# Performance work log

Hardware: AMD Instinct MI355X
Metric: run time of the kernel (lower is better)

Reference implementation:

```python
import jax, jax.numpy as jnp
import numpy as np


def setup_inputs() -> dict:
    key0 = jax.random.key(0)
    k1, k2, k3 = jax.random.split(key0, 3)
    B, T, QS, KS = 64, 4096, 1024, 1024
    query = jax.random.normal(k1, (B, QS), dtype=jnp.float32)
    key = jax.random.normal(k2, (B, T, KS), dtype=jnp.float32)
    mask = jnp.ones((B, T), dtype=jnp.float32)
    # learned params: weights ~ U(-0.1, 0.1), bias zeros
    W = jax.random.uniform(k3, (KS, QS), dtype=jnp.float32) * 0.2 - 0.1
    bias = jnp.zeros((1,), dtype=jnp.float32)
    return {"query": query, "key": key, "mask": mask, "W": W, "bias": bias}


def reference(query, key, mask, W, bias):
    # mids[b] = W @ query[b]  -> [B, KS]
    mids = jnp.einsum("kq,bq->bk", W, query)
    # scores[b,t] = tanh(key[b,t] . mids[b] + bias)  -> [B, T]
    scores = jnp.tanh(jnp.einsum("btk,bk->bt", key, mids) + bias[0])
    # masked softmax over time dim (dim=1)
    scores = scores - jnp.max(scores, axis=1, keepdims=True)
    scores = jnp.exp(scores) * mask
    attn_weights = scores / jnp.sum(scores, axis=1, keepdims=True)
    return attn_weights
```

## Files before the change

### kernel.cpp

```cpp
#include <hip/hip_runtime.h>
#include <math.h>

#define BB 64
#define TT 4096
#define KSZ 1024
#define QSZ 1024

__global__ __launch_bounds__(256) void mids_kernel(const float* __restrict__ query,
                                                   const float* __restrict__ W,
                                                   float* __restrict__ mids) {
    const int bid  = blockIdx.x;
    const int b    = bid >> 6;
    const int kt   = bid & 63;
    const int lane = threadIdx.x & 63;
    const int wave = threadIdx.x >> 6;

    const float4* q4 = (const float4*)(query + (size_t)b * QSZ);
    float4 qr[4];
#pragma unroll
    for (int c = 0; c < 4; ++c) qr[c] = q4[lane + c * 64];

#pragma unroll
    for (int i = 0; i < 4; ++i) {
        const int k = kt * 16 + wave * 4 + i;
        const float4* w4 = (const float4*)(W + (size_t)k * QSZ);
        float sum = 0.f;
#pragma unroll
        for (int c = 0; c < 4; ++c) {
            float4 wv = w4[lane + c * 64];
            sum += wv.x * qr[c].x + wv.y * qr[c].y + wv.z * qr[c].z + wv.w * qr[c].w;
        }
#pragma unroll
        for (int off = 32; off > 0; off >>= 1) sum += __shfl_xor(sum, off, 64);
        if (lane == 0) mids[b * KSZ + k] = sum;
    }
}

__global__ __launch_bounds__(256) void scores_kernel(const float* __restrict__ key,
                                                     const float* __restrict__ mids,
                                                     const float* __restrict__ bias,
                                                     float* __restrict__ scores) {
    const int bid  = blockIdx.x;
    const int b    = bid >> 8;
    const int tt   = bid & 255;
    const int lane = threadIdx.x & 63;
    const int wave = threadIdx.x >> 6;

    const float4* m4 = (const float4*)(mids + (size_t)b * KSZ);
    float4 mr[4];
#pragma unroll
    for (int c = 0; c < 4; ++c) mr[c] = m4[lane + c * 64];
    const float bv = bias[0];

#pragma unroll
    for (int i = 0; i < 4; ++i) {
        const int t = tt * 16 + wave * 4 + i;
        const float4* k4 = (const float4*)(key + ((size_t)b * TT + t) * KSZ);
        float sum = 0.f;
#pragma unroll
        for (int c = 0; c < 4; ++c) {
            float4 kv = k4[lane + c * 64];
            sum += kv.x * mr[c].x + kv.y * mr[c].y + kv.z * mr[c].z + kv.w * mr[c].w;
        }
#pragma unroll
        for (int off = 32; off > 0; off >>= 1) sum += __shfl_xor(sum, off, 64);
        if (lane == 0) scores[b * TT + t] = tanhf(sum + bv);
    }
}

__global__ __launch_bounds__(256) void softmax_kernel(const float* __restrict__ scores,
                                                      const float* __restrict__ mask,
                                                      float* __restrict__ out) {
    const int b    = blockIdx.x;
    const int tid  = threadIdx.x;
    const int lane = tid & 63;
    const int wave = tid >> 6;
    __shared__ float red[8];

    const float4* s4 = (const float4*)(scores + (size_t)b * TT);
    const float4* k4 = (const float4*)(mask + (size_t)b * TT);

    float4 v[4];
#pragma unroll
    for (int c = 0; c < 4; ++c) v[c] = s4[tid + c * 256];

    float mx = -3.0e38f;
#pragma unroll
    for (int c = 0; c < 4; ++c) {
        mx = fmaxf(mx, fmaxf(fmaxf(v[c].x, v[c].y), fmaxf(v[c].z, v[c].w)));
    }
#pragma unroll
    for (int off = 32; off > 0; off >>= 1) mx = fmaxf(mx, __shfl_xor(mx, off, 64));
    if (lane == 0) red[wave] = mx;
    __syncthreads();
    mx = fmaxf(fmaxf(red[0], red[1]), fmaxf(red[2], red[3]));

    float4 e[4];
    float sum = 0.f;
#pragma unroll
    for (int c = 0; c < 4; ++c) {
        float4 mk = k4[tid + c * 256];
        e[c].x = expf(v[c].x - mx) * mk.x;
        e[c].y = expf(v[c].y - mx) * mk.y;
        e[c].z = expf(v[c].z - mx) * mk.z;
        e[c].w = expf(v[c].w - mx) * mk.w;
        sum += e[c].x + e[c].y + e[c].z + e[c].w;
    }
#pragma unroll
    for (int off = 32; off > 0; off >>= 1) sum += __shfl_xor(sum, off, 64);
    if (lane == 0) red[4 + wave] = sum;
    __syncthreads();
    sum = red[4] + red[5] + red[6] + red[7];
    const float inv = 1.0f / sum;

    float4* o4 = (float4*)(out + (size_t)b * TT);
#pragma unroll
    for (int c = 0; c < 4; ++c) {
        float4 o;
        o.x = e[c].x * inv;
        o.y = e[c].y * inv;
        o.z = e[c].z * inv;
        o.w = e[c].w * inv;
        o4[tid + c * 256] = o;
    }
}

extern "C" void kernel_launch(void* const* d_in, const int* in_sizes, int n_in,
                              void* d_out, int out_size, void* d_ws, size_t ws_size,
                              hipStream_t stream) {
    const float* query = (const float*)d_in[0];
    const float* key   = (const float*)d_in[1];
    const float* mask  = (const float*)d_in[2];
    const float* W     = (const float*)d_in[3];
    const float* bias  = (const float*)d_in[4];
    float* out = (float*)d_out;

    float* mids   = (float*)d_ws;
    float* scores = mids + BB * KSZ;

    mids_kernel<<<BB * (KSZ / 16), 256, 0, stream>>>(query, W, mids);
    scores_kernel<<<BB * (TT / 16), 256, 0, stream>>>(key, mids, bias, scores);
    softmax_kernel<<<BB, 256, 0, stream>>>(scores, mask, out);
}
```

Before: 1.322 ms.

## Fuse exp and mask into scores kernel using tanh bound as softmax max

The scores kernel now computes exp(tanh(s)+bias-1)*mask directly. Because tanh is bounded by 1, it uses 1 as a fixed stabilising max in place of the true row max, writes the unnormalised values to the output and stores per-block partial sums. A small norm kernel reduces those partials and rescales the output, which removes the separate max pass and the scores buffer. The mids kernel also swaps its block-index decomposition so consecutive blocks share W rows. The change is mathematically equivalent because the constant shift cancels in normalisation.

```diff
diff --git a/kernel.cpp b/kernel.cpp
--- a/kernel.cpp
+++ b/kernel.cpp
@@ -10,8 +10,8 @@
                                                    const float* __restrict__ W,
                                                    float* __restrict__ mids) {
     const int bid  = blockIdx.x;
-    const int b    = bid >> 6;
-    const int kt   = bid & 63;
+    const int b    = bid & 63;
+    const int kt   = bid >> 6;
     const int lane = threadIdx.x & 63;
     const int wave = threadIdx.x >> 6;
 
@@ -38,13 +38,16 @@
 
 __global__ __launch_bounds__(256) void scores_kernel(const float* __restrict__ key,
                                                      const float* __restrict__ mids,
+                                                     const float* __restrict__ mask,
                                                      const float* __restrict__ bias,
-                                                     float* __restrict__ scores) {
+                                                     float* __restrict__ out,
+                                                     float* __restrict__ partial) {
     const int bid  = blockIdx.x;
     const int b    = bid >> 8;
     const int tt   = bid & 255;
     const int lane = threadIdx.x & 63;
     const int wave = threadIdx.x >> 6;
+    __shared__ float red[4];
 
     const float4* m4 = (const float4*)(mids + (size_t)b * KSZ);
     float4 mr[4];
@@ -52,6 +55,7 @@
     for (int c = 0; c < 4; ++c) mr[c] = m4[lane + c * 64];
     const float bv = bias[0];
 
+    float esum = 0.f;
 #pragma unroll
     for (int i = 0; i < 4; ++i) {
         const int t = tt * 16 + wave * 4 + i;
@@ -64,64 +68,39 @@
         }
 #pragma unroll
         for (int off = 32; off > 0; off >>= 1) sum += __shfl_xor(sum, off, 64);
-        if (lane == 0) scores[b * TT + t] = tanhf(sum + bv);
+        if (lane == 0) {
+            float e = expf(tanhf(sum + bv) - 1.0f) * mask[(size_t)b * TT + t];
+            out[(size_t)b * TT + t] = e;
+            esum += e;
+        }
     }
+    if (lane == 0) red[wave] = esum;
+    __syncthreads();
+    if (threadIdx.x == 0) partial[bid] = (red[0] + red[1]) + (red[2] + red[3]);
 }
 
-__global__ __launch_bounds__(256) void softmax_kernel(const float* __restrict__ scores,
-                                                      const float* __restrict__ mask,
-                                                      float* __restrict__ out) {
+__global__ __launch_bounds__(256) void norm_kernel(const float* __restrict__ partial,
+                                                   float* __restrict__ out) {
     const int b    = blockIdx.x;
     const int tid  = threadIdx.x;
     const int lane = tid & 63;
     const int wave = tid >> 6;
-    __shared__ float red[8];
+    __shared__ float red[4];
 
-    const float4* s4 = (const float4*)(scores + (size_t)b * TT);
-    const float4* k4 = (const float4*)(mask + (size_t)b * TT);
-
-    float4 v[4];
+    float s = partial[b * 256 + tid];
 #pragma unroll
-    for (int c = 0; c < 4; ++c) v[c] = s4[tid + c * 256];
-
-    float mx = -3.0e38f;
-#pragma unroll
-    for (int c = 0; c < 4; ++c) {
-        mx = fmaxf(mx, fmaxf(fmaxf(v[c].x, v[c].y), fmaxf(v[c].z, v[c].w)));
-    }
-#pragma unroll
-    for (int off = 32; off > 0; off >>= 1) mx = fmaxf(mx, __shfl_xor(mx, off, 64));
-    if (lane == 0) red[wave] = mx;
+    for (int off = 32; off > 0; off >>= 1) s += __shfl_xor(s, off, 64);
+    if (lane == 0) red[wave] = s;
     __syncthreads();
-    mx = fmaxf(fmaxf(red[0], red[1]), fmaxf(red[2], red[3]));
-
-    float4 e[4];
-    float sum = 0.f;
-#pragma unroll
-    for (int c = 0; c < 4; ++c) {
-        float4 mk = k4[tid + c * 256];
-        e[c].x = expf(v[c].x - mx) * mk.x;
-        e[c].y = expf(v[c].y - mx) * mk.y;
-        e[c].z = expf(v[c].z - mx) * mk.z;
-        e[c].w = expf(v[c].w - mx) * mk.w;
-        sum += e[c].x + e[c].y + e[c].z + e[c].w;
-    }
-#pragma unroll
-    for (int off = 32; off > 0; off >>= 1) sum += __shfl_xor(sum, off, 64);
-    if (lane == 0) red[4 + wave] = sum;
-    __syncthreads();
-    sum = red[4] + red[5] + red[6] + red[7];
-    const float inv = 1.0f / sum;
+    const float total = (red[0] + red[1]) + (red[2] + red[3]);
+    const float inv = 1.0f / total;
 
     float4* o4 = (float4*)(out + (size_t)b * TT);
 #pragma unroll
     for (int c = 0; c < 4; ++c) {
-        float4 o;
-        o.x = e[c].x * inv;
-        o.y = e[c].y * inv;
-        o.z = e[c].z * inv;
-        o.w = e[c].w * inv;
-        o4[tid + c * 256] = o;
+        float4 v = o4[tid + c * 256];
+        v.x *= inv; v.y *= inv; v.z *= inv; v.w *= inv;
+        o4[tid + c * 256] = v;
     }
 }
 
@@ -135,10 +114,10 @@
     const float* bias  = (const float*)d_in[4];
     float* out = (float*)d_out;
 
-    float* mids   = (float*)d_ws;
-    float* scores = mids + BB * KSZ;
+    float* mids    = (float*)d_ws;
+    float* partial = mids + BB * KSZ;
 
     mids_kernel<<<BB * (KSZ / 16), 256, 0, stream>>>(query, W, mids);
-    scores_kernel<<<BB * (TT / 16), 256, 0, stream>>>(key, mids, bias, scores);
-    softmax_kernel<<<BB, 256, 0, stream>>>(scores, mask, out);
+    scores_kernel<<<BB * (TT / 16), 256, 0, stream>>>(key, mids, mask, bias, out, partial);
+    norm_kernel<<<BB, 256, 0, stream>>>(partial, out);
 }
```

Measured after the change: 1.331 ms. No clear change (+0.7%).
